# Optimization experiments

Hardware: AMD Instinct MI355X
Metric: run time of the kernel (lower is better)

## Reference

```python
import jax, jax.numpy as jnp
import numpy as np
from jax import lax

B, L, C = 128, 200, 300          # batch, text_len, embed_channels
K = 128                          # conv_num_kernel
WS = (2, 3, 4, 5)                # conv_kernel_size
A = 5000                         # num_api
F = 64                           # feature_channels


def setup_inputs() -> dict:
    key = jax.random.key(0)
    ks = jax.random.split(key, 24)
    s = 0.02
    inp = {"x": jax.random.normal(ks[0], (B, L, C), dtype=jnp.float32)}
    for i, ws in enumerate(WS):
        inp[f"conv_w{ws}"] = jax.random.normal(ks[1 + i], (K, C, ws), dtype=jnp.float32) * s
        inp[f"conv_b{ws}"] = jnp.zeros((K,), dtype=jnp.float32)
    D = K * len(WS)
    inp["sc_fcl_w"] = jax.random.normal(ks[5], (A, D), dtype=jnp.float32) * s
    inp["sc_fcl_b"] = jnp.zeros((A,), dtype=jnp.float32)
    inp["fic_fc_w"] = jax.random.normal(ks[6], (F, D), dtype=jnp.float32) * s
    inp["fic_fc_b"] = jnp.zeros((F,), dtype=jnp.float32)
    inp["emb"] = jax.random.uniform(ks[7], (F, A), dtype=jnp.float32)  # torch.rand
    inp["mlp_w1"] = jax.random.normal(ks[8], (F, 2 * F), dtype=jnp.float32) * s
    inp["mlp_b1"] = jnp.zeros((F,), dtype=jnp.float32)
    inp["mlp_w2"] = jax.random.normal(ks[9], (1, F), dtype=jnp.float32) * s
    inp["mlp_b2"] = jnp.zeros((1,), dtype=jnp.float32)
    inp["fic_fcl_w"] = jax.random.normal(ks[10], (A, 2 * A), dtype=jnp.float32) * s
    inp["fic_fcl_b"] = jnp.zeros((A,), dtype=jnp.float32)
    inp["fusion_w"] = jax.random.normal(ks[11], (A, 2 * A), dtype=jnp.float32) * s
    inp["fusion_b"] = jnp.zeros((A,), dtype=jnp.float32)
    inp["task_w"] = jax.random.normal(ks[12], (A, A), dtype=jnp.float32) * s
    inp["task_b"] = jnp.zeros((A,), dtype=jnp.float32)
    return inp


def _textcnn(x_t, conv_ws, conv_bs):
    # x_t: (B, C, L); each branch: conv1d VALID -> relu -> global max over width -> (B, K)
    feats = []
    for w, b in zip(conv_ws, conv_bs):
        y = lax.conv_general_dilated(x_t, w, (1,), 'VALID',
                                     dimension_numbers=('NCH', 'OIH', 'NCH'))
        y = jax.nn.relu(y + b[None, :, None])
        feats.append(jnp.max(y, axis=2))  # full-width max-pool -> (B, K)
    # torch: cat along width dim=2 of (B,K,1) then view(B,-1) -> kernel-window index fastest
    return jnp.stack(feats, axis=2).reshape(x_t.shape[0], -1)  # (B, K*len(WS))


def reference(x, conv_w2, conv_b2, conv_w3, conv_b3, conv_w4, conv_b4,
              conv_w5, conv_b5, sc_fcl_w, sc_fcl_b, fic_fc_w, fic_fc_b, emb,
              mlp_w1, mlp_b1, mlp_w2, mlp_b2, fic_fcl_w, fic_fcl_b,
              fusion_w, fusion_b, task_w, task_b):
    x_t = jnp.transpose(x, (0, 2, 1))  # (B, C, L)
    e = _textcnn(x_t, (conv_w2, conv_w3, conv_w4, conv_w5),
                 (conv_b2, conv_b3, conv_b4, conv_b5))  # (B, D)

    u_sc = e @ sc_fcl_w.T + sc_fcl_b          # (B, A)
    u_sc_trans = e @ fic_fc_w.T + fic_fc_b    # (B, F)
    u_mm = u_sc_trans @ emb                   # (B, A)

    # Batched form of the per-sample repeat/concat + MLP loop:
    # concat(u_rep, emb.T) @ W1.T  ==  u @ W1[:, :F].T (bcast over A) + emb.T @ W1[:, F:].T
    h = (u_sc_trans @ mlp_w1[:, :F].T)[:, None, :] \
        + (emb.T @ mlp_w1[:, F:].T)[None, :, :] + mlp_b1  # (B, A, F)
    u_mlp = jnp.tanh(jnp.einsum('baf,f->ba', h, mlp_w2[0]) + mlp_b2[0])  # (B, A)

    u_fic = jnp.tanh(jnp.concatenate([u_mm, u_mlp], axis=1) @ fic_fcl_w.T + fic_fcl_b)
    u_mmf = jnp.concatenate([u_sc, u_fic], axis=1) @ fusion_w.T + fusion_b
    task = u_mmf @ task_w.T + task_b          # (B, A)
    return task
```

## Files before the change

kernel.cpp:

```cpp
#include <hip/hip_runtime.h>
#include <math.h>

#define B_ 128
#define L_ 200
#define C_ 300
#define K_ 128
#define A_ 5000
#define F_ 64
#define D_ 512
#define CP_ 320
#define LP_ 260
#define NPAD_ 5056
#define KP2_ 10048
#define KP1_ 5056
#define ZMAX_ 12

typedef __attribute__((ext_vector_type(8))) short bf16x8;
typedef __attribute__((ext_vector_type(8))) short short8;
typedef __attribute__((ext_vector_type(4))) float f32x4;

#define MFMA(a,b,c) __builtin_amdgcn_mfma_f32_16x16x32_bf16(a,b,c,0,0,0)

static __device__ __forceinline__ unsigned short f2bf(float f) {
    unsigned u = __float_as_uint(f);
    unsigned r = (u + 0x7FFFu + ((u >> 16) & 1u)) >> 16;
    return (unsigned short)r;
}

#define OFF_XP     ((size_t)0)
#define OFF_WP     ((size_t)5324800)
#define OFF_E      ((size_t)5611520)
#define OFF_EBF    ((size_t)5677056)
#define OFF_UST    ((size_t)5693440)
#define OFF_VB     ((size_t)5701632)
#define OFF_S2     ((size_t)5701696)
#define OFF_UMBF   ((size_t)5701824)
#define OFF_UFBF   ((size_t)6344896)
#define OFF_UMMFBF ((size_t)6987968)
#define OFF_PART   ((size_t)7311552)

__global__ __launch_bounds__(320) void prep_x_kernel(const float* __restrict__ x, short* __restrict__ xp)
{
    const int row = blockIdx.x;
    const int b   = blockIdx.y;
    const int c   = threadIdx.x;
    float v = 0.f;
    if (row < L_ && c < C_) v = x[((size_t)b * L_ + row) * C_ + c];
    xp[((size_t)b * LP_ + row) * CP_ + c] = (short)f2bf(v);
}

__global__ void prep_w_kernel(const float* __restrict__ w2, const float* __restrict__ w3,
                              const float* __restrict__ w4, const float* __restrict__ w5,
                              short* __restrict__ wp)
{
    const int idx = blockIdx.x * 256 + threadIdx.x;
    if (idx >= 128 * 14 * CP_) return;
    int off, wsz; const float* src;
    if (idx < 81920)       { off = idx;          wsz = 2; src = w2; }
    else if (idx < 204800) { off = idx - 81920;  wsz = 3; src = w3; }
    else if (idx < 368640) { off = idx - 204800; wsz = 4; src = w4; }
    else                   { off = idx - 368640; wsz = 5; src = w5; }
    const int k   = off / (wsz * CP_);
    const int r   = off % (wsz * CP_);
    const int tap = r / CP_;
    const int c   = r % CP_;
    float v = 0.f;
    if (c < C_) v = src[((size_t)k * C_ + c) * wsz + tap];
    wp[idx] = (short)f2bf(v);
}

__global__ __launch_bounds__(512) void conv_gemm3_kernel(
    const short* __restrict__ xp, const short* __restrict__ wp,
    const float* __restrict__ b2, const float* __restrict__ b3,
    const float* __restrict__ b4, const float* __restrict__ b5,
    float* __restrict__ e, short* __restrict__ ebf)
{
    const int b  = blockIdx.x;
    const int br = blockIdx.y;
    const int nt = blockIdx.z;
    const int wsz  = br + 2;
    const int Pout = 199 - br;
    const int wbase = (br == 0) ? 0 : (br == 1) ? 81920 : (br == 2) ? 204800 : 368640;

    const int tid  = threadIdx.x;
    const int wave = tid >> 6;
    const int lane = tid & 63;
    const int mw   = wave & 3;
    const int nw   = wave >> 2;

    __shared__ short lA[260 * 36];
    __shared__ short lB[5 * 64 * 36];
    __shared__ float smax[4][64];

    const int nbB = wsz * 256;
    const bool hA2 = (tid < 16);
    const bool hB1 = (tid + 512 < nbB);
    const bool hB2 = (tid + 1024 < nbB);

    const short* xbase = xp + (size_t)b * LP_ * CP_;
    const short* wpb   = wp + wbase + (size_t)(nt * 64) * (wsz * CP_);

    f32x4 acc[4][2];
    #pragma unroll
    for (int mf = 0; mf < 4; ++mf)
        #pragma unroll
        for (int nf = 0; nf < 2; ++nf)
            acc[mf][nf] = (f32x4){0.f, 0.f, 0.f, 0.f};

    short8 a0, a1, a2, bb0, bb1, bb2;

    #define LDA(ch, cc) (*(const short8*)(xbase + (size_t)((ch) >> 2) * CP_ + (cc) * 32 + ((ch) & 3) * 8))
    #define LDB(ch, cc) (*(const short8*)(wpb + (size_t)((((ch) & 255) >> 2)) * (wsz * CP_) + ((ch) >> 8) * CP_ + (cc) * 32 + (((ch) & 255) & 3) * 8))

    a0 = LDA(tid, 0); a1 = LDA(tid + 512, 0);
    if (hA2) a2 = LDA(tid + 1024, 0);
    bb0 = LDB(tid, 0);
    if (hB1) bb1 = LDB(tid + 512, 0);
    if (hB2) bb2 = LDB(tid + 1024, 0);

    for (int cc = 0; cc < 10; ++cc) {
        __syncthreads();
        {
            int ch = tid;        *(short8*)(lA + (ch >> 2) * 36 + (ch & 3) * 8) = a0;
            ch = tid + 512;      *(short8*)(lA + (ch >> 2) * 36 + (ch & 3) * 8) = a1;
            if (hA2) { ch = tid + 1024; *(short8*)(lA + (ch >> 2) * 36 + (ch & 3) * 8) = a2; }
            ch = tid;            *(short8*)(lB + (((ch >> 8) << 6) + ((ch & 255) >> 2)) * 36 + ((ch & 255) & 3) * 8) = bb0;
            if (hB1) { ch = tid + 512;  *(short8*)(lB + (((ch >> 8) << 6) + ((ch & 255) >> 2)) * 36 + ((ch & 255) & 3) * 8) = bb1; }
            if (hB2) { ch = tid + 1024; *(short8*)(lB + (((ch >> 8) << 6) + ((ch & 255) >> 2)) * 36 + ((ch & 255) & 3) * 8) = bb2; }
        }
        __syncthreads();
        if (cc + 1 < 10) {
            a0 = LDA(tid, cc + 1); a1 = LDA(tid + 512, cc + 1);
            if (hA2) a2 = LDA(tid + 1024, cc + 1);
            bb0 = LDB(tid, cc + 1);
            if (hB1) bb1 = LDB(tid + 512, cc + 1);
            if (hB2) bb2 = LDB(tid + 1024, cc + 1);
        }
        for (int tap = 0; tap < wsz; ++tap) {
            bf16x8 af[4], bfr[2];
            #pragma unroll
            for (int mf = 0; mf < 4; ++mf)
                af[mf] = *(const bf16x8*)(lA + (mw * 64 + mf * 16 + (lane & 15) + tap) * 36 + (lane >> 4) * 8);
            #pragma unroll
            for (int nf = 0; nf < 2; ++nf)
                bfr[nf] = *(const bf16x8*)(lB + (tap * 64 + nw * 32 + nf * 16 + (lane & 15)) * 36 + (lane >> 4) * 8);
            #pragma unroll
            for (int mf = 0; mf < 4; ++mf)
                #pragma unroll
                for (int nf = 0; nf < 2; ++nf)
                    acc[mf][nf] = MFMA(af[mf], bfr[nf], acc[mf][nf]);
        }
    }
    #undef LDA
    #undef LDB

    float vm0 = -1e30f, vm1 = -1e30f;
    #pragma unroll
    for (int mf = 0; mf < 4; ++mf) {
        const int rowbase = mw * 64 + mf * 16 + (lane >> 4) * 4;
        #pragma unroll
        for (int r = 0; r < 4; ++r) {
            const bool valid = (rowbase + r) < Pout;
            vm0 = fmaxf(vm0, valid ? acc[mf][0][r] : -1e30f);
            vm1 = fmaxf(vm1, valid ? acc[mf][1][r] : -1e30f);
        }
    }
    vm0 = fmaxf(vm0, __shfl_xor(vm0, 16)); vm0 = fmaxf(vm0, __shfl_xor(vm0, 32));
    vm1 = fmaxf(vm1, __shfl_xor(vm1, 16)); vm1 = fmaxf(vm1, __shfl_xor(vm1, 32));
    if (lane < 16) {
        smax[mw][nw * 32 + lane]      = vm0;
        smax[mw][nw * 32 + 16 + lane] = vm1;
    }
    __syncthreads();
    if (tid < 64) {
        const float m = fmaxf(fmaxf(smax[0][tid], smax[1][tid]), fmaxf(smax[2][tid], smax[3][tid]));
        const int k = nt * 64 + tid;
        const float* bp = (br == 0) ? b2 : (br == 1) ? b3 : (br == 2) ? b4 : b5;
        const float val = fmaxf(bp[k] + m, 0.f);
        e[(size_t)b * D_ + k * 4 + br] = val;
        ebf[(size_t)b * D_ + k * 4 + br] = (short)f2bf(val);
    }
}

__global__ __launch_bounds__(512) void gemm3_kernel(
    const short* __restrict__ Abf, int Kpad,
    const float* __restrict__ W, int K, int N,
    int steps_per_z, float* __restrict__ partial)
{
    const int n0 = blockIdx.x * 64;
    const int total = Kpad >> 6;
    const int sbeg = blockIdx.y * steps_per_z;
    const int send = min(sbeg + steps_per_z, total);

    const int tid  = threadIdx.x;
    const int wave = tid >> 6;
    const int lane = tid & 63;
    const int mw   = wave & 3;
    const int nw   = wave >> 2;

    __shared__ short lA[128 * 68];
    __shared__ short lB[64 * 68];

    const int arow = tid >> 2, ac0 = (tid & 3) * 16;
    const int fil  = tid >> 3, wc0 = (tid & 7) * 8;

    f32x4 acc[2][2];
    #pragma unroll
    for (int mf = 0; mf < 2; ++mf)
        #pragma unroll
        for (int nf = 0; nf < 2; ++nf)
            acc[mf][nf] = (f32x4){0.f, 0.f, 0.f, 0.f};

    short8 ra0, ra1;
    float4 rw0, rw1;
    const bool wrow_ok = (n0 + fil) < N;

    {
        const int kb = sbeg * 64;
        ra0 = *(const short8*)(Abf + (size_t)arow * Kpad + kb + ac0);
        ra1 = *(const short8*)(Abf + (size_t)arow * Kpad + kb + ac0 + 8);
        rw0 = make_float4(0.f,0.f,0.f,0.f); rw1 = rw0;
        if (wrow_ok && (kb + wc0) < K)     rw0 = *(const float4*)(W + (size_t)(n0 + fil) * K + kb + wc0);
        if (wrow_ok && (kb + wc0 + 4) < K) rw1 = *(const float4*)(W + (size_t)(n0 + fil) * K + kb + wc0 + 4);
    }

    for (int s = sbeg; s < send; ++s) {
        __syncthreads();
        *(short8*)(lA + arow * 68 + ac0)     = ra0;
        *(short8*)(lA + arow * 68 + ac0 + 8) = ra1;
        {
            short8 wb;
            wb[0]=(short)f2bf(rw0.x); wb[1]=(short)f2bf(rw0.y); wb[2]=(short)f2bf(rw0.z); wb[3]=(short)f2bf(rw0.w);
            wb[4]=(short)f2bf(rw1.x); wb[5]=(short)f2bf(rw1.y); wb[6]=(short)f2bf(rw1.z); wb[7]=(short)f2bf(rw1.w);
            *(short8*)(lB + fil * 68 + wc0) = wb;
        }
        __syncthreads();
        if (s + 1 < send) {
            const int kb = (s + 1) * 64;
            ra0 = *(const short8*)(Abf + (size_t)arow * Kpad + kb + ac0);
            ra1 = *(const short8*)(Abf + (size_t)arow * Kpad + kb + ac0 + 8);
            float4 t0 = make_float4(0.f,0.f,0.f,0.f), t1 = t0;
            if (wrow_ok && (kb + wc0) < K)     t0 = *(const float4*)(W + (size_t)(n0 + fil) * K + kb + wc0);
            if (wrow_ok && (kb + wc0 + 4) < K) t1 = *(const float4*)(W + (size_t)(n0 + fil) * K + kb + wc0 + 4);
            rw0 = t0; rw1 = t1;
        }
        #pragma unroll
        for (int ks = 0; ks < 2; ++ks) {
            bf16x8 af[2], bfr[2];
            #pragma unroll
            for (int mf = 0; mf < 2; ++mf)
                af[mf] = *(const bf16x8*)(lA + (mw * 32 + mf * 16 + (lane & 15)) * 68 + ks * 32 + (lane >> 4) * 8);
            #pragma unroll
            for (int nf = 0; nf < 2; ++nf)
                bfr[nf] = *(const bf16x8*)(lB + (nw * 32 + nf * 16 + (lane & 15)) * 68 + ks * 32 + (lane >> 4) * 8);
            #pragma unroll
            for (int mf = 0; mf < 2; ++mf)
                #pragma unroll
                for (int nf = 0; nf < 2; ++nf)
                    acc[mf][nf] = MFMA(af[mf], bfr[nf], acc[mf][nf]);
        }
    }

    #pragma unroll
    for (int mf = 0; mf < 2; ++mf)
        #pragma unroll
        for (int nf = 0; nf < 2; ++nf)
            #pragma unroll
            for (int r = 0; r < 4; ++r) {
                const int row = mw * 32 + mf * 16 + (lane >> 4) * 4 + r;
                const int col = nw * 32 + nf * 16 + (lane & 15);
                partial[((size_t)blockIdx.y * B_ + row) * NPAD_ + n0 + col] = acc[mf][nf][r];
            }
}

__global__ void reduce2_kernel(const float* __restrict__ partial, const float* __restrict__ bias,
                               float* __restrict__ outf, short* __restrict__ outb,
                               int N, int ldo, int ooff, int js, int act, int padn)
{
    const int Ntot = N + padn;
    const int idx = blockIdx.x * 256 + threadIdx.x;
    if (idx >= B_ * Ntot) return;
    const int n = idx % Ntot;
    const int b = idx / Ntot;
    if (n >= N) { outb[(size_t)b * ldo + ooff + n] = 0; return; }
    float s = bias[n];
    for (int k = 0; k < js; ++k) s += partial[((size_t)k * B_ + b) * NPAD_ + n];
    if (act) s = tanhf(s);
    if (outb) outb[(size_t)b * ldo + ooff + n] = (short)f2bf(s);
    else      outf[(size_t)b * ldo + ooff + n] = s;
}

__global__ __launch_bounds__(256) void ust_kernel(
    const float* __restrict__ e, const float* __restrict__ W,
    const float* __restrict__ bias, float* __restrict__ ust)
{
    const int b = blockIdx.x;
    const int f = threadIdx.x >> 2;
    const int q = threadIdx.x & 3;
    const float* er = e + (size_t)b * D_ + q * 128;
    const float* wr = W + (size_t)f * D_ + q * 128;
    float acc = 0.f;
    #pragma unroll
    for (int j = 0; j < 128; j += 4) {
        const float4 ev = *(const float4*)(er + j);
        const float4 wv = *(const float4*)(wr + j);
        acc += ev.x*wv.x + ev.y*wv.y + ev.z*wv.z + ev.w*wv.w;
    }
    acc += __shfl_xor(acc, 1);
    acc += __shfl_xor(acc, 2);
    if (q == 0) ust[(size_t)b * F_ + f] = acc + bias[f];
}

__global__ void prep_kernel(const float* __restrict__ mlp_w1, const float* __restrict__ mlp_b1,
                            const float* __restrict__ mlp_w2, const float* __restrict__ mlp_b2,
                            const float* __restrict__ ust,
                            float* __restrict__ vB, float* __restrict__ s2)
{
    __shared__ float vA[64];
    __shared__ float csh;
    const int tid = threadIdx.x;
    if (tid < 64) {
        float a = 0.f;
        for (int f = 0; f < 64; ++f) a += mlp_w2[f] * mlp_w1[f * 128 + tid];
        vA[tid] = a;
    } else {
        const int g = tid - 64;
        float bsum = 0.f;
        for (int f = 0; f < 64; ++f) bsum += mlp_w2[f] * mlp_w1[f * 128 + 64 + g];
        vB[g] = bsum;
    }
    if (tid == 0) {
        float c = mlp_b2[0];
        for (int f = 0; f < 64; ++f) c += mlp_b1[f] * mlp_w2[f];
        csh = c;
    }
    __syncthreads();
    float s = csh;
    const float* ub = ust + (size_t)tid * F_;
    for (int g = 0; g < 64; ++g) s += ub[g] * vA[g];
    s2[tid] = s;
}

__global__ void um3_kernel(const float* __restrict__ ust, const float* __restrict__ emb,
                           const float* __restrict__ s2, const float* __restrict__ vB,
                           short* __restrict__ umb)
{
    const int b = blockIdx.y;
    __shared__ float us[64];
    __shared__ float vb[64];
    if (threadIdx.x < 64) {
        us[threadIdx.x] = ust[(size_t)b * F_ + threadIdx.x];
        vb[threadIdx.x] = vB[threadIdx.x];
    }
    __syncthreads();
    const int a = blockIdx.x * 256 + threadIdx.x;
    if (a < A_) {
        float accm = 0.f, acct = 0.f;
        #pragma unroll
        for (int g = 0; g < 64; ++g) {
            const float ev = emb[(size_t)g * A_ + a];
            accm += us[g] * ev;
            acct += vb[g] * ev;
        }
        umb[(size_t)b * KP2_ + a] = (short)f2bf(accm);
        umb[(size_t)b * KP2_ + A_ + a] = (short)f2bf(tanhf(s2[b] + acct));
    } else if (a < A_ + 48) {
        umb[(size_t)b * KP2_ + A_ + a] = 0;
    }
}

extern "C" void kernel_launch(void* const* d_in, const int* in_sizes, int n_in,
                              void* d_out, int out_size, void* d_ws, size_t ws_size,
                              hipStream_t stream)
{
    const float* x       = (const float*)d_in[0];
    const float* conv_w2 = (const float*)d_in[1];
    const float* conv_b2 = (const float*)d_in[2];
    const float* conv_w3 = (const float*)d_in[3];
    const float* conv_b3 = (const float*)d_in[4];
    const float* conv_w4 = (const float*)d_in[5];
    const float* conv_b4 = (const float*)d_in[6];
    const float* conv_w5 = (const float*)d_in[7];
    const float* conv_b5 = (const float*)d_in[8];
    const float* sc_fcl_w = (const float*)d_in[9];
    const float* sc_fcl_b = (const float*)d_in[10];
    const float* fic_fc_w = (const float*)d_in[11];
    const float* fic_fc_b = (const float*)d_in[12];
    const float* emb      = (const float*)d_in[13];
    const float* mlp_w1   = (const float*)d_in[14];
    const float* mlp_b1   = (const float*)d_in[15];
    const float* mlp_w2   = (const float*)d_in[16];
    const float* mlp_b2   = (const float*)d_in[17];
    const float* fic_fcl_w = (const float*)d_in[18];
    const float* fic_fcl_b = (const float*)d_in[19];
    const float* fusion_w  = (const float*)d_in[20];
    const float* fusion_b  = (const float*)d_in[21];
    const float* task_w    = (const float*)d_in[22];
    const float* task_b    = (const float*)d_in[23];

    float* ws = (float*)d_ws;
    short* xp     = (short*)(ws + OFF_XP);
    short* wp     = (short*)(ws + OFF_WP);
    float* e      = ws + OFF_E;
    short* ebf    = (short*)(ws + OFF_EBF);
    float* ust    = ws + OFF_UST;
    float* vB     = ws + OFF_VB;
    float* s2     = ws + OFF_S2;
    short* umbf   = (short*)(ws + OFF_UMBF);
    short* ufbf   = (short*)(ws + OFF_UFBF);
    short* ummfbf = (short*)(ws + OFF_UMMFBF);
    float* part   = ws + OFF_PART;
    float* out    = (float*)d_out;

    prep_x_kernel<<<dim3(LP_, B_), CP_, 0, stream>>>(x, xp);
    prep_w_kernel<<<(128*14*CP_ + 255)/256, 256, 0, stream>>>(conv_w2, conv_w3, conv_w4, conv_w5, wp);

    conv_gemm3_kernel<<<dim3(B_, 4, 2), 512, 0, stream>>>(xp, wp, conv_b2, conv_b3, conv_b4, conv_b5, e, ebf);

    gemm3_kernel<<<dim3(79, 4), 512, 0, stream>>>(ebf, D_, sc_fcl_w, D_, A_, 2, part);
    reduce2_kernel<<<(B_*A_ + 255)/256, 256, 0, stream>>>(part, sc_fcl_b, nullptr, ufbf, A_, KP2_, 0, 4, 0, 0);

    ust_kernel<<<B_, 256, 0, stream>>>(e, fic_fc_w, fic_fc_b, ust);

    prep_kernel<<<1, 128, 0, stream>>>(mlp_w1, mlp_b1, mlp_w2, mlp_b2, ust, vB, s2);
    um3_kernel<<<dim3(20, B_), 256, 0, stream>>>(ust, emb, s2, vB, umbf);

    gemm3_kernel<<<dim3(79, 12), 512, 0, stream>>>(umbf, KP2_, fic_fcl_w, 2*A_, A_, 14, part);
    reduce2_kernel<<<(B_*(A_+48) + 255)/256, 256, 0, stream>>>(part, fic_fcl_b, nullptr, ufbf, A_, KP2_, A_, 12, 1, 48);

    gemm3_kernel<<<dim3(79, 12), 512, 0, stream>>>(ufbf, KP2_, fusion_w, 2*A_, A_, 14, part);
    reduce2_kernel<<<(B_*(A_+56) + 255)/256, 256, 0, stream>>>(part, fusion_b, nullptr, ummfbf, A_, KP1_, 0, 12, 0, 56);

    gemm3_kernel<<<dim3(79, 12), 512, 0, stream>>>(ummfbf, KP1_, task_w, A_, A_, 7, part);
    reduce2_kernel<<<(B_*A_ + 255)/256, 256, 0, stream>>>(part, task_b, out, nullptr, A_, A_, 0, 12, 0, 0);
}
```

Before: 315.6 us.

## Restructure conv GEMM into templated per-branch body with larger per-wave tiles

Replaces the conv kernel, which split the 128 output channels across two blocks of 512 threads, with one 256-thread block per (batch, branch). Each wave now computes an 8x4 fragment tile covering all 128 channels, and the window size becomes a template parameter so the tap and load loops fully unroll. The LDS row layout changes to a 32-element stride with an 8-element pad every four rows. This removes the duplicated staging of the input tile across the two channel blocks and the runtime-bounded tap loop. In exchange it halves the grid to 512 blocks and raises accumulator register pressure, which may lower occupancy.

```diff
diff --git a/kernel.cpp b/kernel.cpp
--- a/kernel.cpp
+++ b/kernel.cpp
@@ -13,13 +13,14 @@
 #define NPAD_ 5056
 #define KP2_ 10048
 #define KP1_ 5056
-#define ZMAX_ 12
 
 typedef __attribute__((ext_vector_type(8))) short bf16x8;
 typedef __attribute__((ext_vector_type(8))) short short8;
 typedef __attribute__((ext_vector_type(4))) float f32x4;
 
 #define MFMA(a,b,c) __builtin_amdgcn_mfma_f32_16x16x32_bf16(a,b,c,0,0,0)
+
+#define ROFF(r) ((r)*32 + ((r)>>2)*8)
 
 static __device__ __forceinline__ unsigned short f2bf(float f) {
     unsigned u = __float_as_uint(f);
@@ -69,117 +70,130 @@
     wp[idx] = (short)f2bf(v);
 }
 
-__global__ __launch_bounds__(512) void conv_gemm3_kernel(
+template<int WSZ>
+__device__ __forceinline__ void conv_body(
+    const short* __restrict__ xbase, const short* __restrict__ wpb,
+    const float* __restrict__ bp, float* __restrict__ e, short* __restrict__ ebf,
+    int b, int br, short* lA, short* lB, float (*smax)[128])
+{
+    const int Pout = 199 - br;
+    const int tid  = threadIdx.x;
+    const int wave = tid >> 6;
+    const int lane = tid & 63;
+    const int mw   = wave & 1;
+    const int nw   = wave >> 1;
+
+    f32x4 acc[8][4];
+    #pragma unroll
+    for (int mf = 0; mf < 8; ++mf)
+        #pragma unroll
+        for (int nf = 0; nf < 4; ++nf)
+            acc[mf][nf] = (f32x4){0.f, 0.f, 0.f, 0.f};
+
+    short8 aR[5];
+    short8 bR[2 * WSZ];
+
+    #define LDA4(ch, cc) (*(const short8*)(xbase + (size_t)((ch) >> 2) * CP_ + (cc) * 32 + ((ch) & 3) * 8))
+    #define LDB4(ch, cc) (*(const short8*)(wpb + (size_t)(((ch) >> 2) & 127) * (WSZ * CP_) + (((ch) >> 2) >> 7) * CP_ + (cc) * 32 + ((ch) & 3) * 8))
+
+    #pragma unroll
+    for (int k = 0; k < 5; ++k) {
+        const int ch = tid + k * 256;
+        if (k < 4 || ch < 1040) aR[k] = LDA4(ch, 0);
+    }
+    #pragma unroll
+    for (int k = 0; k < 2 * WSZ; ++k) bR[k] = LDB4(tid + k * 256, 0);
+
+    for (int cc = 0; cc < 10; ++cc) {
+        __syncthreads();
+        #pragma unroll
+        for (int k = 0; k < 5; ++k) {
+            const int ch = tid + k * 256;
+            if (k < 4 || ch < 1040)
+                *(short8*)(lA + ROFF(ch >> 2) + (ch & 3) * 8) = aR[k];
+        }
+        #pragma unroll
+        for (int k = 0; k < 2 * WSZ; ++k) {
+            const int ch = tid + k * 256;
+            *(short8*)(lB + ROFF(ch >> 2) + (ch & 3) * 8) = bR[k];
+        }
+        __syncthreads();
+        if (cc + 1 < 10) {
+            #pragma unroll
+            for (int k = 0; k < 5; ++k) {
+                const int ch = tid + k * 256;
+                if (k < 4 || ch < 1040) aR[k] = LDA4(ch, cc + 1);
+            }
+            #pragma unroll
+            for (int k = 0; k < 2 * WSZ; ++k) bR[k] = LDB4(tid + k * 256, cc + 1);
+        }
+        #pragma unroll
+        for (int tap = 0; tap < WSZ; ++tap) {
+            bf16x8 bfr[4];
+            #pragma unroll
+            for (int nf = 0; nf < 4; ++nf)
+                bfr[nf] = *(const bf16x8*)(lB + ROFF(tap * 128 + nw * 64 + nf * 16 + (lane & 15)) + (lane >> 4) * 8);
+            #pragma unroll
+            for (int mf = 0; mf < 8; ++mf) {
+                const bf16x8 af = *(const bf16x8*)(lA + ROFF(mw * 128 + mf * 16 + (lane & 15) + tap) + (lane >> 4) * 8);
+                #pragma unroll
+                for (int nf = 0; nf < 4; ++nf)
+                    acc[mf][nf] = MFMA(af, bfr[nf], acc[mf][nf]);
+            }
+        }
+    }
+    #undef LDA4
+    #undef LDB4
+
+    float vm[4] = {-1e30f, -1e30f, -1e30f, -1e30f};
+    #pragma unroll
+    for (int mf = 0; mf < 8; ++mf) {
+        const int rowbase = mw * 128 + mf * 16 + (lane >> 4) * 4;
+        #pragma unroll
+        for (int r = 0; r < 4; ++r) {
+            const bool valid = (rowbase + r) < Pout;
+            #pragma unroll
+            for (int nf = 0; nf < 4; ++nf)
+                vm[nf] = fmaxf(vm[nf], valid ? acc[mf][nf][r] : -1e30f);
+        }
+    }
+    #pragma unroll
+    for (int nf = 0; nf < 4; ++nf) {
+        vm[nf] = fmaxf(vm[nf], __shfl_xor(vm[nf], 16));
+        vm[nf] = fmaxf(vm[nf], __shfl_xor(vm[nf], 32));
+    }
+    if (lane < 16) {
+        #pragma unroll
+        for (int nf = 0; nf < 4; ++nf)
+            smax[mw][nw * 64 + nf * 16 + lane] = vm[nf];
+    }
+    __syncthreads();
+    if (tid < 128) {
+        const float m = fmaxf(smax[0][tid], smax[1][tid]);
+        const float val = fmaxf(bp[tid] + m, 0.f);
+        e[(size_t)b * D_ + tid * 4 + br] = val;
+        ebf[(size_t)b * D_ + tid * 4 + br] = (short)f2bf(val);
+    }
+}
+
+__global__ __launch_bounds__(256) void conv_gemm4_kernel(
     const short* __restrict__ xp, const short* __restrict__ wp,
     const float* __restrict__ b2, const float* __restrict__ b3,
     const float* __restrict__ b4, const float* __restrict__ b5,
     float* __restrict__ e, short* __restrict__ ebf)
 {
+    __shared__ short lA[8832];
+    __shared__ short lB[21752];
+    __shared__ float smax[2][128];
+
     const int b  = blockIdx.x;
     const int br = blockIdx.y;
-    const int nt = blockIdx.z;
-    const int wsz  = br + 2;
-    const int Pout = 199 - br;
-    const int wbase = (br == 0) ? 0 : (br == 1) ? 81920 : (br == 2) ? 204800 : 368640;
-
-    const int tid  = threadIdx.x;
-    const int wave = tid >> 6;
-    const int lane = tid & 63;
-    const int mw   = wave & 3;
-    const int nw   = wave >> 2;
-
-    __shared__ short lA[260 * 36];
-    __shared__ short lB[5 * 64 * 36];
-    __shared__ float smax[4][64];
-
-    const int nbB = wsz * 256;
-    const bool hA2 = (tid < 16);
-    const bool hB1 = (tid + 512 < nbB);
-    const bool hB2 = (tid + 1024 < nbB);
-
     const short* xbase = xp + (size_t)b * LP_ * CP_;
-    const short* wpb   = wp + wbase + (size_t)(nt * 64) * (wsz * CP_);
-
-    f32x4 acc[4][2];
-    #pragma unroll
-    for (int mf = 0; mf < 4; ++mf)
-        #pragma unroll
-        for (int nf = 0; nf < 2; ++nf)
-            acc[mf][nf] = (f32x4){0.f, 0.f, 0.f, 0.f};
-
-    short8 a0, a1, a2, bb0, bb1, bb2;
-
-    #define LDA(ch, cc) (*(const short8*)(xbase + (size_t)((ch) >> 2) * CP_ + (cc) * 32 + ((ch) & 3) * 8))
-    #define LDB(ch, cc) (*(const short8*)(wpb + (size_t)((((ch) & 255) >> 2)) * (wsz * CP_) + ((ch) >> 8) * CP_ + (cc) * 32 + (((ch) & 255) & 3) * 8))
-
-    a0 = LDA(tid, 0); a1 = LDA(tid + 512, 0);
-    if (hA2) a2 = LDA(tid + 1024, 0);
-    bb0 = LDB(tid, 0);
-    if (hB1) bb1 = LDB(tid + 512, 0);
-    if (hB2) bb2 = LDB(tid + 1024, 0);
-
-    for (int cc = 0; cc < 10; ++cc) {
-        __syncthreads();
-        {
-            int ch = tid;        *(short8*)(lA + (ch >> 2) * 36 + (ch & 3) * 8) = a0;
-            ch = tid + 512;      *(short8*)(lA + (ch >> 2) * 36 + (ch & 3) * 8) = a1;
-            if (hA2) { ch = tid + 1024; *(short8*)(lA + (ch >> 2) * 36 + (ch & 3) * 8) = a2; }
-            ch = tid;            *(short8*)(lB + (((ch >> 8) << 6) + ((ch & 255) >> 2)) * 36 + ((ch & 255) & 3) * 8) = bb0;
-            if (hB1) { ch = tid + 512;  *(short8*)(lB + (((ch >> 8) << 6) + ((ch & 255) >> 2)) * 36 + ((ch & 255) & 3) * 8) = bb1; }
-            if (hB2) { ch = tid + 1024; *(short8*)(lB + (((ch >> 8) << 6) + ((ch & 255) >> 2)) * 36 + ((ch & 255) & 3) * 8) = bb2; }
-        }
-        __syncthreads();
-        if (cc + 1 < 10) {
-            a0 = LDA(tid, cc + 1); a1 = LDA(tid + 512, cc + 1);
-            if (hA2) a2 = LDA(tid + 1024, cc + 1);
-            bb0 = LDB(tid, cc + 1);
-            if (hB1) bb1 = LDB(tid + 512, cc + 1);
-            if (hB2) bb2 = LDB(tid + 1024, cc + 1);
-        }
-        for (int tap = 0; tap < wsz; ++tap) {
-            bf16x8 af[4], bfr[2];
-            #pragma unroll
-            for (int mf = 0; mf < 4; ++mf)
-                af[mf] = *(const bf16x8*)(lA + (mw * 64 + mf * 16 + (lane & 15) + tap) * 36 + (lane >> 4) * 8);
-            #pragma unroll
-            for (int nf = 0; nf < 2; ++nf)
-                bfr[nf] = *(const bf16x8*)(lB + (tap * 64 + nw * 32 + nf * 16 + (lane & 15)) * 36 + (lane >> 4) * 8);
-            #pragma unroll
-            for (int mf = 0; mf < 4; ++mf)
-                #pragma unroll
-                for (int nf = 0; nf < 2; ++nf)
-                    acc[mf][nf] = MFMA(af[mf], bfr[nf], acc[mf][nf]);
-        }
-    }
-    #undef LDA
-    #undef LDB
-
-    float vm0 = -1e30f, vm1 = -1e30f;
-    #pragma unroll
-    for (int mf = 0; mf < 4; ++mf) {
-        const int rowbase = mw * 64 + mf * 16 + (lane >> 4) * 4;
-        #pragma unroll
-        for (int r = 0; r < 4; ++r) {
-            const bool valid = (rowbase + r) < Pout;
-            vm0 = fmaxf(vm0, valid ? acc[mf][0][r] : -1e30f);
-            vm1 = fmaxf(vm1, valid ? acc[mf][1][r] : -1e30f);
-        }
-    }
-    vm0 = fmaxf(vm0, __shfl_xor(vm0, 16)); vm0 = fmaxf(vm0, __shfl_xor(vm0, 32));
-    vm1 = fmaxf(vm1, __shfl_xor(vm1, 16)); vm1 = fmaxf(vm1, __shfl_xor(vm1, 32));
-    if (lane < 16) {
-        smax[mw][nw * 32 + lane]      = vm0;
-        smax[mw][nw * 32 + 16 + lane] = vm1;
-    }
-    __syncthreads();
-    if (tid < 64) {
-        const float m = fmaxf(fmaxf(smax[0][tid], smax[1][tid]), fmaxf(smax[2][tid], smax[3][tid]));
-        const int k = nt * 64 + tid;
-        const float* bp = (br == 0) ? b2 : (br == 1) ? b3 : (br == 2) ? b4 : b5;
-        const float val = fmaxf(bp[k] + m, 0.f);
-        e[(size_t)b * D_ + k * 4 + br] = val;
-        ebf[(size_t)b * D_ + k * 4 + br] = (short)f2bf(val);
-    }
+
+    if (br == 0)      conv_body<2>(xbase, wp,          b2, e, ebf, b, 0, lA, lB, smax);
+    else if (br == 1) conv_body<3>(xbase, wp + 81920,  b3, e, ebf, b, 1, lA, lB, smax);
+    else if (br == 2) conv_body<4>(xbase, wp + 204800, b4, e, ebf, b, 2, lA, lB, smax);
+    else              conv_body<5>(xbase, wp + 368640, b5, e, ebf, b, 3, lA, lB, smax);
 }
 
 __global__ __launch_bounds__(512) void gemm3_kernel(
@@ -415,7 +429,7 @@
     prep_x_kernel<<<dim3(LP_, B_), CP_, 0, stream>>>(x, xp);
     prep_w_kernel<<<(128*14*CP_ + 255)/256, 256, 0, stream>>>(conv_w2, conv_w3, conv_w4, conv_w5, wp);
 
-    conv_gemm3_kernel<<<dim3(B_, 4, 2), 512, 0, stream>>>(xp, wp, conv_b2, conv_b3, conv_b4, conv_b5, e, ebf);
+    conv_gemm4_kernel<<<dim3(B_, 4), 256, 0, stream>>>(xp, wp, conv_b2, conv_b3, conv_b4, conv_b5, e, ebf);
 
     gemm3_kernel<<<dim3(79, 4), 512, 0, stream>>>(ebf, D_, sc_fcl_w, D_, A_, 2, part);
     reduce2_kernel<<<(B_*A_ + 255)/256, 256, 0, stream>>>(part, sc_fcl_b, nullptr, ufbf, A_, KP2_, 0, 4, 0, 0);
```

After: 317.6 us. No clear change (+0.6%).
